# Optimization experiments

Measured on AMD Instinct MI355X. Metric: run time of the kernel, lower is better.

Reference implementation:

```python
import jax, jax.numpy as jnp
import numpy as np

NUM_EMBEDDINGS = 1024
EMBEDDING_DIM = 128
COMMITMENT_COST = 0.25


def setup_inputs() -> dict:
    key = jax.random.key(0)
    k1, k2 = jax.random.split(key)
    z = jax.random.normal(k1, (16, EMBEDDING_DIM, 64, 64), dtype=jnp.float32)
    # torch init: uniform(-1/num_embeddings, 1/num_embeddings)
    lim = 1.0 / NUM_EMBEDDINGS
    embedding = jax.random.uniform(
        k2, (NUM_EMBEDDINGS, EMBEDDING_DIM), dtype=jnp.float32,
        minval=-lim, maxval=lim)
    return {"z": z, "embedding": embedding}


def reference(z, embedding):
    b, c, h, w = z.shape  # c == EMBEDDING_DIM
    # (b, h, w, c) -> (b*h*w, c)
    z_flat = jnp.transpose(z, (0, 2, 3, 1)).reshape(-1, c)
    # squared euclidean distances: ||z||^2 + ||e||^2 - 2 z e^T  -> (N, K)
    distances = (jnp.sum(z_flat ** 2, axis=-1, keepdims=True)
                 + jnp.sum(embedding ** 2, axis=-1)[None, :]
                 - 2.0 * jnp.matmul(z_flat, embedding.T))
    encoding_indices = jnp.argmin(distances, axis=-1)  # (N,) int
    z_q = embedding[encoding_indices].reshape(b, h, w, c)
    z_q = jnp.transpose(z_q, (0, 3, 1, 2))  # (b, c, h, w)
    commitment_loss = COMMITMENT_COST * jnp.sum(
        (jax.lax.stop_gradient(z_q) - z) ** 2)
    codebook_loss = jnp.sum((z_q - jax.lax.stop_gradient(z)) ** 2)
    loss = codebook_loss + commitment_loss
    # straight-through estimator
    z_q_st = z + jax.lax.stop_gradient(z_q - z)
    return (z_q_st, loss, encoding_indices, commitment_loss, codebook_loss)
```

## Files before the change

### kernel.cpp

```cpp
#include <hip/hip_runtime.h>
#include <hip/hip_bf16.h>

#define C 128
#define HW 4096
#define NPOS 65536
#define K 1024
#define MB 128
#define NBLK (NPOS/MB)
#define RS 136
#define RSB 272
#define CHK 64
#define NCH (K/CHK)
#define CHB (CHK*RSB)

#define ZQ_OFF 0
#define LOSS_OFF 8388608
#define IDX_OFF 8388609
#define COMMIT_OFF 8454145
#define CODE_OFF 8454146

#define WS_IMG_OFF 8192

typedef __bf16 bf16x8 __attribute__((ext_vector_type(8)));
typedef float f32x4 __attribute__((ext_vector_type(4)));

__global__ void vq_prep(const float* __restrict__ emb, unsigned char* __restrict__ img) {
    int k = blockIdx.x;
    int l = threadIdx.x;
    float v0 = emb[k * C + l];
    float v1 = emb[k * C + 64 + l];
    __hip_bfloat16 h0 = __float2bfloat16(v0);
    __hip_bfloat16 h1 = __float2bfloat16(v1);
    unsigned short* row = (unsigned short*)(img + (size_t)k * RSB);
    row[l] = *(unsigned short*)&h0;
    row[64 + l] = *(unsigned short*)&h1;
    float s = v0 * v0 + v1 * v1;
    #pragma unroll
    for (int off = 32; off; off >>= 1) s += __shfl_down(s, off);
    if (l == 0) *(float*)(img + (size_t)k * RSB + 256) = s + 1.0f;
}

__global__ __launch_bounds__(256, 2)
void vq_main(const float* __restrict__ z, const float* __restrict__ emb,
             const unsigned char* __restrict__ img,
             float* __restrict__ out, float* __restrict__ S) {
    __shared__ unsigned short zt[MB * RS];
    __shared__ unsigned short bbuf[2][CHK * RS];
    __shared__ unsigned int wbest[4][MB];
    __shared__ unsigned short idxs[MB];
    __shared__ float lred[4];

    const int t = threadIdx.x;
    const int w = t >> 6;
    const int lane = t & 63;
    const int nn = lane & 15;
    const int q = lane >> 4;

    const int blk = blockIdx.x;
    const int n0g = blk * MB;
    const int b = n0g >> 12;
    const int hw0 = n0g & (HW - 1);
    const float* zg = z + (size_t)b * C * HW + hw0;

    for (int j = w; j < 17; j += 4) {
        __builtin_amdgcn_global_load_lds(
            (const __attribute__((address_space(1))) unsigned int*)(img + j * 1024 + lane * 16),
            (__attribute__((address_space(3))) unsigned int*)((unsigned char*)bbuf[0] + j * 1024),
            16, 0, 0);
    }

    {
        int pos = t & (MB - 1);
        int c0b = (t >> 7) * 64;
        #pragma unroll
        for (int i = 0; i < 16; ++i) {
            int c0 = c0b + i * 4;
            float f0 = zg[(size_t)(c0 + 0) * HW + pos];
            float f1 = zg[(size_t)(c0 + 1) * HW + pos];
            float f2 = zg[(size_t)(c0 + 2) * HW + pos];
            float f3 = zg[(size_t)(c0 + 3) * HW + pos];
            __hip_bfloat16 h0 = __float2bfloat16(f0), h1 = __float2bfloat16(f1),
                           h2 = __float2bfloat16(f2), h3 = __float2bfloat16(f3);
            ushort4 pk;
            pk.x = *(unsigned short*)&h0; pk.y = *(unsigned short*)&h1;
            pk.z = *(unsigned short*)&h2; pk.w = *(unsigned short*)&h3;
            *(ushort4*)&zt[pos * RS + c0] = pk;
        }
    }
    __syncthreads();

    bf16x8 a[8][4];
    #pragma unroll
    for (int mt = 0; mt < 8; ++mt)
        #pragma unroll
        for (int ks = 0; ks < 4; ++ks)
            a[mt][ks] = *(bf16x8*)&zt[(mt * 16 + nn) * RS + ks * 32 + q * 8];

    unsigned int best[8][4];
    #pragma unroll
    for (int mt = 0; mt < 8; ++mt)
        #pragma unroll
        for (int r = 0; r < 4; ++r) best[mt][r] = 0xFFFFFFFFu;

    for (int ch = 0; ch < NCH; ++ch) {
        const int p = ch & 1;
        if (ch + 1 < NCH) {
            const unsigned char* src = img + (size_t)(ch + 1) * CHB;
            for (int j = w; j < 17; j += 4) {
                __builtin_amdgcn_global_load_lds(
                    (const __attribute__((address_space(1))) unsigned int*)(src + j * 1024 + lane * 16),
                    (__attribute__((address_space(3))) unsigned int*)((unsigned char*)bbuf[p ^ 1] + j * 1024),
                    16, 0, 0);
            }
        }
        const unsigned short* bb = bbuf[p];
        const int row = w * 16 + nn;
        bf16x8 bf[4];
        #pragma unroll
        for (int ks = 0; ks < 4; ++ks)
            bf[ks] = *(bf16x8*)&bb[row * RS + ks * 32 + q * 8];
        const float en1 = *(const float*)&bb[row * RS + 128];
        const unsigned int code = (unsigned int)(ch * CHK + row);

        f32x4 acc[8];
        #pragma unroll
        for (int mt = 0; mt < 8; ++mt) acc[mt] = (f32x4){0.f, 0.f, 0.f, 0.f};
        #pragma unroll
        for (int ks = 0; ks < 4; ++ks)
            #pragma unroll
            for (int mt = 0; mt < 8; ++mt)
                acc[mt] = __builtin_amdgcn_mfma_f32_16x16x32_bf16(a[mt][ks], bf[ks], acc[mt], 0, 0, 0);

        #pragma unroll
        for (int mt = 0; mt < 8; ++mt)
            #pragma unroll
            for (int r = 0; r < 4; ++r) {
                float s = fmaf(acc[mt][r], -2.0f, en1);
                unsigned int u = (__float_as_uint(s) & ~1023u) | code;
                best[mt][r] = min(best[mt][r], u);
            }
        __syncthreads();
    }

    #pragma unroll
    for (int mt = 0; mt < 8; ++mt)
        #pragma unroll
        for (int r = 0; r < 4; ++r) {
            unsigned int v = best[mt][r];
            v = min(v, (unsigned int)__shfl_xor((int)v, 1));
            v = min(v, (unsigned int)__shfl_xor((int)v, 2));
            v = min(v, (unsigned int)__shfl_xor((int)v, 4));
            v = min(v, (unsigned int)__shfl_xor((int)v, 8));
            if (nn == 0) wbest[w][mt * 16 + q * 4 + r] = v;
        }
    __syncthreads();

    if (t < MB) {
        unsigned int v = min(min(wbest[0][t], wbest[1][t]), min(wbest[2][t], wbest[3][t]));
        unsigned int code = v & 1023u;
        idxs[t] = (unsigned short)code;
        out[IDX_OFF + n0g + t] = (float)code;
    }
    __syncthreads();

    {
        int pos = t & (MB - 1);
        int c0b = (t >> 7) * 64;
        int myidx = idxs[pos];
        const float* erow = emb + (size_t)myidx * C;
        float* og = out + ZQ_OFF + (size_t)b * C * HW + hw0;
        float ls = 0.f;
        #pragma unroll
        for (int i = 0; i < 16; ++i) {
            int c0 = c0b + i * 4;
            float4 ev = *(const float4*)&erow[c0];
            ushort4 zz = *(ushort4*)&zt[pos * RS + c0];
            float z0 = __uint_as_float((unsigned int)zz.x << 16);
            float z1 = __uint_as_float((unsigned int)zz.y << 16);
            float z2 = __uint_as_float((unsigned int)zz.z << 16);
            float z3 = __uint_as_float((unsigned int)zz.w << 16);
            float d0 = z0 - ev.x, d1 = z1 - ev.y, d2 = z2 - ev.z, d3 = z3 - ev.w;
            ls += d0 * d0 + d1 * d1 + d2 * d2 + d3 * d3;
            og[(size_t)(c0 + 0) * HW + pos] = ev.x;
            og[(size_t)(c0 + 1) * HW + pos] = ev.y;
            og[(size_t)(c0 + 2) * HW + pos] = ev.z;
            og[(size_t)(c0 + 3) * HW + pos] = ev.w;
        }
        #pragma unroll
        for (int off = 32; off; off >>= 1) ls += __shfl_down(ls, off);
        if (lane == 0) lred[w] = ls;
    }
    __syncthreads();
    if (t == 0) atomicAdd(S, lred[0] + lred[1] + lred[2] + lred[3]);
}

__global__ void vq_final(const float* __restrict__ S, float* __restrict__ out) {
    float s = *S;
    out[LOSS_OFF] = 1.25f * s;
    out[COMMIT_OFF] = 0.25f * s;
    out[CODE_OFF] = s;
}

extern "C" void kernel_launch(void* const* d_in, const int* in_sizes, int n_in,
                              void* d_out, int out_size, void* d_ws, size_t ws_size,
                              hipStream_t stream) {
    const float* z = (const float*)d_in[0];
    const float* emb = (const float*)d_in[1];
    float* out = (float*)d_out;
    float* S = (float*)d_ws;
    unsigned char* img = (unsigned char*)d_ws + WS_IMG_OFF;

    hipMemsetAsync(d_ws, 0, 64, stream);
    vq_prep<<<K, 64, 0, stream>>>(emb, img);
    vq_main<<<NBLK, 256, 0, stream>>>(z, emb, img, out, S);
    vq_final<<<1, 1, 0, stream>>>(S, out);
}
```

Before: 116.6 us.

## Load codebook fragments directly from global into registers, fuse finalize into main

The main kernel no longer stages codebook chunks through double-buffered LDS with async global-to-LDS copies and a per-chunk barrier. Each lane now loads its B fragment and norm straight from global memory into registers, prefetching one chunk ahead, and the row stride is padded. The memset and the final reduction kernel are also removed: zeroing moves into the prep kernel, and the last block to arrive on a counter writes the losses. This cuts barriers, LDS use and launch overhead, at the cost of relying on L2/cache hit rates for the repeated codebook reads.

```diff
diff --git a/kernel.cpp b/kernel.cpp
--- a/kernel.cpp
+++ b/kernel.cpp
@@ -8,7 +8,7 @@
 #define MB 128
 #define NBLK (NPOS/MB)
 #define RS 136
-#define RSB 272
+#define RSB 320
 #define CHK 64
 #define NCH (K/CHK)
 #define CHB (CHK*RSB)
@@ -24,9 +24,11 @@
 typedef __bf16 bf16x8 __attribute__((ext_vector_type(8)));
 typedef float f32x4 __attribute__((ext_vector_type(4)));
 
-__global__ void vq_prep(const float* __restrict__ emb, unsigned char* __restrict__ img) {
+__global__ void vq_prep(const float* __restrict__ emb, unsigned char* __restrict__ img,
+                        float* __restrict__ S) {
     int k = blockIdx.x;
     int l = threadIdx.x;
+    if (k == 0 && l == 0) { S[0] = 0.0f; ((unsigned int*)S)[1] = 0u; }
     float v0 = emb[k * C + l];
     float v1 = emb[k * C + 64 + l];
     __hip_bfloat16 h0 = __float2bfloat16(v0);
@@ -45,7 +47,6 @@
              const unsigned char* __restrict__ img,
              float* __restrict__ out, float* __restrict__ S) {
     __shared__ unsigned short zt[MB * RS];
-    __shared__ unsigned short bbuf[2][CHK * RS];
     __shared__ unsigned int wbest[4][MB];
     __shared__ unsigned short idxs[MB];
     __shared__ float lred[4];
@@ -61,13 +62,6 @@
     const int b = n0g >> 12;
     const int hw0 = n0g & (HW - 1);
     const float* zg = z + (size_t)b * C * HW + hw0;
-
-    for (int j = w; j < 17; j += 4) {
-        __builtin_amdgcn_global_load_lds(
-            (const __attribute__((address_space(1))) unsigned int*)(img + j * 1024 + lane * 16),
-            (__attribute__((address_space(3))) unsigned int*)((unsigned char*)bbuf[0] + j * 1024),
-            16, 0, 0);
-    }
 
     {
         int pos = t & (MB - 1);
@@ -102,24 +96,23 @@
         #pragma unroll
         for (int r = 0; r < 4; ++r) best[mt][r] = 0xFFFFFFFFu;
 
+    const int row = w * 16 + nn;
+    const unsigned char* pb = img + (size_t)row * RSB + q * 16;
+    const unsigned char* pe = img + (size_t)row * RSB + 256;
+
+    bf16x8 bcur[4];
+    #pragma unroll
+    for (int ks = 0; ks < 4; ++ks) bcur[ks] = *(const bf16x8*)(pb + ks * 64);
+    float ecur = *(const float*)pe;
+
+    #pragma unroll 2
     for (int ch = 0; ch < NCH; ++ch) {
-        const int p = ch & 1;
-        if (ch + 1 < NCH) {
-            const unsigned char* src = img + (size_t)(ch + 1) * CHB;
-            for (int j = w; j < 17; j += 4) {
-                __builtin_amdgcn_global_load_lds(
-                    (const __attribute__((address_space(1))) unsigned int*)(src + j * 1024 + lane * 16),
-                    (__attribute__((address_space(3))) unsigned int*)((unsigned char*)bbuf[p ^ 1] + j * 1024),
-                    16, 0, 0);
-            }
-        }
-        const unsigned short* bb = bbuf[p];
-        const int row = w * 16 + nn;
-        bf16x8 bf[4];
-        #pragma unroll
-        for (int ks = 0; ks < 4; ++ks)
-            bf[ks] = *(bf16x8*)&bb[row * RS + ks * 32 + q * 8];
-        const float en1 = *(const float*)&bb[row * RS + 128];
+        const int step = (ch + 1 < NCH) ? CHB : 0;
+        bf16x8 bnxt[4];
+        #pragma unroll
+        for (int ks = 0; ks < 4; ++ks) bnxt[ks] = *(const bf16x8*)(pb + step + ks * 64);
+        float enxt = *(const float*)(pe + step);
+
         const unsigned int code = (unsigned int)(ch * CHK + row);
 
         f32x4 acc[8];
@@ -129,17 +122,21 @@
         for (int ks = 0; ks < 4; ++ks)
             #pragma unroll
             for (int mt = 0; mt < 8; ++mt)
-                acc[mt] = __builtin_amdgcn_mfma_f32_16x16x32_bf16(a[mt][ks], bf[ks], acc[mt], 0, 0, 0);
+                acc[mt] = __builtin_amdgcn_mfma_f32_16x16x32_bf16(a[mt][ks], bcur[ks], acc[mt], 0, 0, 0);
 
         #pragma unroll
         for (int mt = 0; mt < 8; ++mt)
             #pragma unroll
             for (int r = 0; r < 4; ++r) {
-                float s = fmaf(acc[mt][r], -2.0f, en1);
+                float s = fmaf(acc[mt][r], -2.0f, ecur);
                 unsigned int u = (__float_as_uint(s) & ~1023u) | code;
                 best[mt][r] = min(best[mt][r], u);
             }
-        __syncthreads();
+
+        #pragma unroll
+        for (int ks = 0; ks < 4; ++ks) bcur[ks] = bnxt[ks];
+        ecur = enxt;
+        pb += CHB; pe += CHB;
     }
 
     #pragma unroll
@@ -191,14 +188,20 @@
         if (lane == 0) lred[w] = ls;
     }
     __syncthreads();
-    if (t == 0) atomicAdd(S, lred[0] + lred[1] + lred[2] + lred[3]);
-}
-
-__global__ void vq_final(const float* __restrict__ S, float* __restrict__ out) {
-    float s = *S;
-    out[LOSS_OFF] = 1.25f * s;
-    out[COMMIT_OFF] = 0.25f * s;
-    out[CODE_OFF] = s;
+
+    if (t == 0) {
+        float bs = lred[0] + lred[1] + lred[2] + lred[3];
+        atomicAdd(S, bs);
+        __threadfence();
+        unsigned int old = atomicAdd((unsigned int*)S + 1, 1u);
+        if (old == NBLK - 1) {
+            __threadfence();
+            float s = atomicAdd(S, 0.0f);
+            out[LOSS_OFF] = 1.25f * s;
+            out[COMMIT_OFF] = 0.25f * s;
+            out[CODE_OFF] = s;
+        }
+    }
 }
 
 extern "C" void kernel_launch(void* const* d_in, const int* in_sizes, int n_in,
@@ -210,8 +213,6 @@
     float* S = (float*)d_ws;
     unsigned char* img = (unsigned char*)d_ws + WS_IMG_OFF;
 
-    hipMemsetAsync(d_ws, 0, 64, stream);
-    vq_prep<<<K, 64, 0, stream>>>(emb, img);
+    vq_prep<<<K, 64, 0, stream>>>(emb, img, S);
     vq_main<<<NBLK, 256, 0, stream>>>(z, emb, img, out, S);
-    vq_final<<<1, 1, 0, stream>>>(S, out);
 }
```

Result: slower. 135.1 us (+15.9%).

## Retile MFMA warps to 2x2 grid and fold accumulator reset into prep kernel

Applied to the files above, without the earlier changes.

Warps are rearranged from each covering all 128 positions against 16 codes into a 2x2 layout where each covers 64 positions against 32 codes. This halves the A-fragment registers per warp and cuts the shared-memory traffic per MFMA, and the cross-warp argmin reduction now spans two warps instead of four. Separately, the hipMemsetAsync that zeroed the loss accumulator is dropped and the zeroing moves into vq_prep, removing one launch from the stream.

```diff
diff --git a/kernel.cpp b/kernel.cpp
--- a/kernel.cpp
+++ b/kernel.cpp
@@ -24,9 +24,11 @@
 typedef __bf16 bf16x8 __attribute__((ext_vector_type(8)));
 typedef float f32x4 __attribute__((ext_vector_type(4)));
 
-__global__ void vq_prep(const float* __restrict__ emb, unsigned char* __restrict__ img) {
+__global__ void vq_prep(const float* __restrict__ emb, unsigned char* __restrict__ img,
+                        float* __restrict__ S) {
     int k = blockIdx.x;
     int l = threadIdx.x;
+    if (k == 0 && l == 0) S[0] = 0.0f;
     float v0 = emb[k * C + l];
     float v1 = emb[k * C + 64 + l];
     __hip_bfloat16 h0 = __float2bfloat16(v0);
@@ -46,7 +48,7 @@
              float* __restrict__ out, float* __restrict__ S) {
     __shared__ unsigned short zt[MB * RS];
     __shared__ unsigned short bbuf[2][CHK * RS];
-    __shared__ unsigned int wbest[4][MB];
+    __shared__ unsigned int wbest[2][MB];
     __shared__ unsigned short idxs[MB];
     __shared__ float lred[4];
 
@@ -55,6 +57,8 @@
     const int lane = t & 63;
     const int nn = lane & 15;
     const int q = lane >> 4;
+    const int wm = w >> 1;
+    const int wn = w & 1;
 
     const int blk = blockIdx.x;
     const int n0g = blk * MB;
@@ -89,16 +93,16 @@
     }
     __syncthreads();
 
-    bf16x8 a[8][4];
-    #pragma unroll
-    for (int mt = 0; mt < 8; ++mt)
+    bf16x8 a[4][4];
+    #pragma unroll
+    for (int mt = 0; mt < 4; ++mt)
         #pragma unroll
         for (int ks = 0; ks < 4; ++ks)
-            a[mt][ks] = *(bf16x8*)&zt[(mt * 16 + nn) * RS + ks * 32 + q * 8];
-
-    unsigned int best[8][4];
-    #pragma unroll
-    for (int mt = 0; mt < 8; ++mt)
+            a[mt][ks] = *(bf16x8*)&zt[(wm * 64 + mt * 16 + nn) * RS + ks * 32 + q * 8];
+
+    unsigned int best[4][4];
+    #pragma unroll
+    for (int mt = 0; mt < 4; ++mt)
         #pragma unroll
         for (int r = 0; r < 4; ++r) best[mt][r] = 0xFFFFFFFFu;
 
@@ -114,36 +118,47 @@
             }
         }
         const unsigned short* bb = bbuf[p];
-        const int row = w * 16 + nn;
-        bf16x8 bf[4];
+
+        bf16x8 bf[2][4];
+        float en[2];
+        #pragma unroll
+        for (int nt = 0; nt < 2; ++nt) {
+            const int row = wn * 32 + nt * 16 + nn;
+            #pragma unroll
+            for (int ks = 0; ks < 4; ++ks)
+                bf[nt][ks] = *(bf16x8*)&bb[row * RS + ks * 32 + q * 8];
+            en[nt] = *(const float*)&bb[row * RS + 128];
+        }
+        const unsigned int code0 = (unsigned int)(ch * CHK + wn * 32 + nn);
+
+        f32x4 acc[4][2];
+        #pragma unroll
+        for (int mt = 0; mt < 4; ++mt)
+            #pragma unroll
+            for (int nt = 0; nt < 2; ++nt) acc[mt][nt] = (f32x4){0.f, 0.f, 0.f, 0.f};
         #pragma unroll
         for (int ks = 0; ks < 4; ++ks)
-            bf[ks] = *(bf16x8*)&bb[row * RS + ks * 32 + q * 8];
-        const float en1 = *(const float*)&bb[row * RS + 128];
-        const unsigned int code = (unsigned int)(ch * CHK + row);
-
-        f32x4 acc[8];
-        #pragma unroll
-        for (int mt = 0; mt < 8; ++mt) acc[mt] = (f32x4){0.f, 0.f, 0.f, 0.f};
-        #pragma unroll
-        for (int ks = 0; ks < 4; ++ks)
-            #pragma unroll
-            for (int mt = 0; mt < 8; ++mt)
-                acc[mt] = __builtin_amdgcn_mfma_f32_16x16x32_bf16(a[mt][ks], bf[ks], acc[mt], 0, 0, 0);
-
-        #pragma unroll
-        for (int mt = 0; mt < 8; ++mt)
+            #pragma unroll
+            for (int mt = 0; mt < 4; ++mt)
+                #pragma unroll
+                for (int nt = 0; nt < 2; ++nt)
+                    acc[mt][nt] = __builtin_amdgcn_mfma_f32_16x16x32_bf16(a[mt][ks], bf[nt][ks], acc[mt][nt], 0, 0, 0);
+
+        #pragma unroll
+        for (int mt = 0; mt < 4; ++mt)
             #pragma unroll
             for (int r = 0; r < 4; ++r) {
-                float s = fmaf(acc[mt][r], -2.0f, en1);
-                unsigned int u = (__float_as_uint(s) & ~1023u) | code;
-                best[mt][r] = min(best[mt][r], u);
+                float s0 = fmaf(acc[mt][0][r], -2.0f, en[0]);
+                float s1 = fmaf(acc[mt][1][r], -2.0f, en[1]);
+                unsigned int u0 = (__float_as_uint(s0) & ~1023u) | code0;
+                unsigned int u1 = (__float_as_uint(s1) & ~1023u) | (code0 + 16u);
+                best[mt][r] = min(best[mt][r], min(u0, u1));
             }
         __syncthreads();
     }
 
     #pragma unroll
-    for (int mt = 0; mt < 8; ++mt)
+    for (int mt = 0; mt < 4; ++mt)
         #pragma unroll
         for (int r = 0; r < 4; ++r) {
             unsigned int v = best[mt][r];
@@ -151,12 +166,12 @@
             v = min(v, (unsigned int)__shfl_xor((int)v, 2));
             v = min(v, (unsigned int)__shfl_xor((int)v, 4));
             v = min(v, (unsigned int)__shfl_xor((int)v, 8));
-            if (nn == 0) wbest[w][mt * 16 + q * 4 + r] = v;
+            if (nn == 0) wbest[wn][wm * 64 + mt * 16 + q * 4 + r] = v;
         }
     __syncthreads();
 
     if (t < MB) {
-        unsigned int v = min(min(wbest[0][t], wbest[1][t]), min(wbest[2][t], wbest[3][t]));
+        unsigned int v = min(wbest[0][t], wbest[1][t]);
         unsigned int code = v & 1023u;
         idxs[t] = (unsigned short)code;
         out[IDX_OFF + n0g + t] = (float)code;
@@ -210,8 +225,7 @@
     float* S = (float*)d_ws;
     unsigned char* img = (unsigned char*)d_ws + WS_IMG_OFF;
 
-    hipMemsetAsync(d_ws, 0, 64, stream);
-    vq_prep<<<K, 64, 0, stream>>>(emb, img);
+    vq_prep<<<K, 64, 0, stream>>>(emb, img, S);
     vq_main<<<NBLK, 256, 0, stream>>>(z, emb, img, out, S);
     vq_final<<<1, 1, 0, stream>>>(S, out);
 }
```

Result: no change. 115.2 us (-1.2%).
